# Performance work log

Measured on AMD Instinct MI355X. Metric: run time of the kernel, lower is better.

The kernel has to match this reference:

```python
import jax, jax.numpy as jnp
import numpy as np

LEAK = 0.01  # torch LeakyReLU default negative_slope

def lrelu(x):
    return jnp.where(x >= 0, x, LEAK * x)

def edge_conv(x, src, dst, ea, W1, b1, W2, b2):
    # message: cat(x_i=target, x_j=source, edge_attr) -> Linear -> LeakyReLU -> Linear
    m = jnp.concatenate([x[dst], x[src], ea], axis=1)          # [E, 2F+Fe]
    h = lrelu(m @ W1 + b1) @ W2 + b2                            # [E, H]
    n = x.shape[0]
    agg = jnp.full((n, h.shape[1]), jnp.inf, h.dtype).at[dst].min(h)  # scatter-min at target
    return jnp.where(jnp.isfinite(agg), agg, jnp.zeros_like(agg))     # empty nodes -> 0


def setup_inputs() -> dict:
    key = jax.random.key(0)
    ks = jax.random.split(key, 20)
    B, N, E = 4, 20000, 640000
    NF, AD, EF, H = 2, 1, 1, 8
    inp = {
        "node_features": jax.random.randint(ks[0], (B, N, NF), 0, 10, dtype=jnp.int32),
        "actions": jax.random.normal(ks[1], (B, N), dtype=jnp.float32),
        "edge_index": jax.random.randint(ks[2], (B, 2, E), 0, N, dtype=jnp.int64),
        "edge_features": jax.random.normal(ks[3], (B, E, EF), dtype=jnp.float32),
    }
    d0 = NF + AD  # 3
    def lin(k, fin, fout):
        s = 1.0 / np.sqrt(fin)
        k1, k2 = jax.random.split(k)
        return (jax.random.uniform(k1, (fin, fout), jnp.float32, -s, s),
                jax.random.uniform(k2, (fout,), jnp.float32, -s, s))
    inp["c1_W1"], inp["c1_b1"] = lin(ks[4], 2 * d0 + EF, H)
    inp["c1_W2"], inp["c1_b2"] = lin(ks[5], H, H)
    inp["c2_W1"], inp["c2_b1"] = lin(ks[6], 2 * H + 1, H)
    inp["c2_W2"], inp["c2_b2"] = lin(ks[7], H, H)
    inp["c3_W1"], inp["c3_b1"] = lin(ks[8], 2 * H + 1, H)
    inp["c3_W2"], inp["c3_b2"] = lin(ks[9], H, H)
    inp["lin_W"], inp["lin_b"] = lin(ks[10], d0 + H, 1)
    return inp


def reference(node_features, actions, edge_index, edge_features,
              c1_W1, c1_b1, c1_W2, c1_b2,
              c2_W1, c2_b1, c2_W2, c2_b2,
              c3_W1, c3_b1, c3_W2, c3_b2,
              lin_W, lin_b):
    # x = int(node_features) concat actions  -> float
    x0 = jnp.concatenate([node_features.astype(jnp.int32).astype(jnp.float32),
                          actions[..., None]], axis=-1)  # [B,N,3]

    def per_graph(x0g, eig, eag):
        src, dst = eig[0], eig[1]  # flow source_to_target: x_j=src, x_i=dst
        h = lrelu(edge_conv(x0g, src, dst, eag, c1_W1, c1_b1, c1_W2, c1_b2))
        h = lrelu(edge_conv(h, src, dst, eag, c2_W1, c2_b1, c2_W2, c2_b2))
        h = lrelu(edge_conv(h, src, dst, eag, c3_W1, c3_b1, c3_W2, c3_b2))
        xc = jnp.concatenate([x0g, h], axis=1)  # [N, 3+8]
        return jnp.sum(xc, axis=0)              # sum-pool over nodes

    pooled = jax.vmap(per_graph)(x0, edge_index, edge_features)  # [B, 11]
    return pooled @ lin_W + lin_b  # [B, 1]
```

## Files before the change

kernel.cpp:

```cpp
#include <hip/hip_runtime.h>

#define LEAK 0.01f
#define BS 128
#define PCHUNK 4096
#define PT 512
#define CT 256
#define MAXNB 256
#define CPGMAX 256

__device__ __forceinline__ float lrelu(float v) {
    return v >= 0.f ? v : LEAK * v;
}

__device__ __forceinline__ unsigned int fmin_encode(float x) {
    unsigned int u = __float_as_uint(x);
    return (u & 0x80000000u) ? ~u : (u | 0x80000000u);
}
__device__ __forceinline__ float fmin_decode(unsigned int k) {
    unsigned int u = (k & 0x80000000u) ? (k ^ 0x80000000u) : ~k;
    return __uint_as_float(u);
}

__device__ __forceinline__ void block_add(float c, float* dst) {
    __shared__ float wsum[8];
#pragma unroll
    for (int off = 32; off > 0; off >>= 1) c += __shfl_down(c, off, 64);
    int lane = threadIdx.x & 63;
    int wave = threadIdx.x >> 6;
    if (lane == 0) wsum[wave] = c;
    __syncthreads();
    if (threadIdx.x == 0) {
        float s = 0.f;
        int nw = blockDim.x >> 6;
        for (int w = 0; w < nw; ++w) s += wsum[w];
        atomicAdd(dst, s);
    }
}

__global__ __launch_bounds__(PT) void part_init_kernel(
    const int* __restrict__ ei, const float* __restrict__ ea,
    int2* __restrict__ pairs, int* __restrict__ ofs,
    const int* __restrict__ nf, const float* __restrict__ act,
    const float* __restrict__ W1, const float* __restrict__ b1,
    const float* __restrict__ lw, const float* __restrict__ lb,
    float* __restrict__ a1, float* __restrict__ a2, float* __restrict__ out,
    int E, int N, int NB, int CPG) {
    int b = blockIdx.y;
    int t = threadIdx.x;

    if (blockIdx.x >= CPG) {
        int n = (blockIdx.x - CPG) * PT + t;
        float c = 0.f;
        if (n < N) {
            size_t i = (size_t)b * N + n;
            float x0 = (float)nf[i * 2 + 0];
            float x1 = (float)nf[i * 2 + 1];
            float x2 = act[i];
            float v1[8], v2[8];
#pragma unroll
            for (int j = 0; j < 8; ++j) {
                v1[j] = b1[j] + x0 * W1[0 * 8 + j] + x1 * W1[1 * 8 + j] + x2 * W1[2 * 8 + j];
                v2[j] =         x0 * W1[3 * 8 + j] + x1 * W1[4 * 8 + j] + x2 * W1[5 * 8 + j];
            }
            float4* o1 = (float4*)(a1 + i * 8);
            float4* o2 = (float4*)(a2 + i * 8);
            o1[0] = make_float4(v1[0], v1[1], v1[2], v1[3]);
            o1[1] = make_float4(v1[4], v1[5], v1[6], v1[7]);
            o2[0] = make_float4(v2[0], v2[1], v2[2], v2[3]);
            o2[1] = make_float4(v2[4], v2[5], v2[6], v2[7]);
            c = x0 * lw[0] + x1 * lw[1] + x2 * lw[2];
            if (n == 0) c += lb[0];
        }
        block_add(c, &out[b]);
        return;
    }

    __shared__ int lc[MAXNB];
    __shared__ int lofs[MAXNB + 1];
    __shared__ int ts[PT];
    int c = blockIdx.x;
    for (int i = t; i < NB; i += PT) lc[i] = 0;
    __syncthreads();

    int e0 = c * PCHUNK;
    int end = min(e0 + PCHUNK, E);
    const int* srow = ei + (size_t)b * 2 * E;
    const int* drow = srow + E;

    int pk[PCHUNK / PT];
#pragma unroll
    for (int j = 0; j < PCHUNK / PT; ++j) {
        int e = e0 + j * PT + t;
        int p = -1;
        if (e < end) {
            int d = drow[e];
            int bin = d >> 7;
            int r = atomicAdd(&lc[bin], 1);
            p = bin | ((d & 127) << 10) | (r << 17);
        }
        pk[j] = p;
    }
    __syncthreads();

    int v = (t < NB) ? lc[t] : 0;
    ts[t] = v;
    __syncthreads();
    int incl = v;
    for (int off = 1; off < PT; off <<= 1) {
        int add = (t >= off) ? ts[t - off] : 0;
        __syncthreads();
        incl += add;
        ts[t] = incl;
        __syncthreads();
    }
    if (t < NB) lofs[t] = incl - v;
    if (t == PT - 1) lofs[NB] = incl;
    __syncthreads();

    for (int i = t; i <= NB; i += PT) {
        int w = lofs[i];
        ofs[((size_t)b * (NB + 1) + i) * CPG + c] = w;
        if (i < NB) lc[i] = w;
    }
    __syncthreads();

    size_t pbase = (size_t)b * E + e0;
#pragma unroll
    for (int j = 0; j < PCHUNK / PT; ++j) {
        int e = e0 + j * PT + t;
        if (e < end) {
            int p = pk[j];
            int bin = p & 1023;
            int dl = (p >> 10) & 127;
            int r = p >> 17;
            int pos = lc[bin] + r;
            pairs[pbase + pos] =
                make_int2(srow[e] | (dl << 16), __float_as_int(ea[(size_t)b * E + e]));
        }
    }
}


__device__ __forceinline__ void conv_edge_body(
    const float* __restrict__ a2g, const float* we, const float* bb,
    const float* __restrict__ W2, int2 p,
    const float* __restrict__ a1s, unsigned int* __restrict__ acc) {
    int srcn = p.x & 0xFFFF;
    int dl = (p.x >> 16) & 127;
    float eav = __int_as_float(p.y);
    const float4* q = (const float4*)(a2g + (size_t)srcn * 8);
    float4 lo = q[0], hi = q[1];
    float h1[8];
    h1[0] = a1s[dl * 9 + 0] + lo.x; h1[1] = a1s[dl * 9 + 1] + lo.y;
    h1[2] = a1s[dl * 9 + 2] + lo.z; h1[3] = a1s[dl * 9 + 3] + lo.w;
    h1[4] = a1s[dl * 9 + 4] + hi.x; h1[5] = a1s[dl * 9 + 5] + hi.y;
    h1[6] = a1s[dl * 9 + 6] + hi.z; h1[7] = a1s[dl * 9 + 7] + hi.w;
#pragma unroll
    for (int j = 0; j < 8; ++j) {
        h1[j] = fmaf(eav, we[j], h1[j]);
        h1[j] = lrelu(h1[j]);
    }
    float h2[8];
#pragma unroll
    for (int j = 0; j < 8; ++j) h2[j] = bb[j];
#pragma unroll
    for (int kk = 0; kk < 8; ++kk) {
        float hk = h1[kk];
#pragma unroll
        for (int j = 0; j < 8; ++j) h2[j] = fmaf(hk, W2[kk * 8 + j], h2[j]);
    }
#pragma unroll
    for (int j = 0; j < 8; ++j)
        atomicMin(&acc[dl * 9 + j], fmin_encode(h2[j]));
}

__device__ __forceinline__ void conv_edges_runs(
    const float* __restrict__ a2g, const float* we, const float* bb,
    const float* __restrict__ W2, const int2* __restrict__ pairsg,
    const int* __restrict__ ofb, int CPG,
    const float* __restrict__ a1s, unsigned int* __restrict__ acc,
    int* __restrict__ rs, int* __restrict__ re) {
    int t = threadIdx.x;
    for (int c = t; c < CPG; c += CT) {
        rs[c] = ofb[c];
        re[c] = ofb[CPG + c];
    }
    __syncthreads();
    int sw = t >> 5, sub = t & 31;
    const int nsw = CT >> 5;
    int c = sw;
    int2 pcur = make_int2(0, 0);
    int kcur = 0, k1cur = 0;
    if (c < CPG) {
        int cb = c * PCHUNK;
        kcur = cb + rs[c] + sub;
        k1cur = cb + re[c];
        if (kcur < k1cur) pcur = pairsg[kcur];
    }
    while (c < CPG) {
        int cn = c + nsw;
        int2 pnext = make_int2(0, 0);
        int knext = 0, k1next = 0;
        if (cn < CPG) {
            int cb = cn * PCHUNK;
            knext = cb + rs[cn] + sub;
            k1next = cb + re[cn];
            if (knext < k1next) pnext = pairsg[knext];
        }
        if (kcur < k1cur) {
            conv_edge_body(a2g, we, bb, W2, pcur, a1s, acc);
            for (int k = kcur + 32; k < k1cur; k += 32)
                conv_edge_body(a2g, we, bb, W2, pairsg[k], a1s, acc);
        }
        c = cn; kcur = knext; k1cur = k1next; pcur = pnext;
    }
}

__global__ __launch_bounds__(CT) void conv_mid_kernel(
    const float* __restrict__ a1, const float* __restrict__ a2,
    const float* __restrict__ w1e, const float* __restrict__ W2,
    const float* __restrict__ b2,
    const float* __restrict__ nW1, const float* __restrict__ nb1,
    const int* __restrict__ ofs, const int2* __restrict__ pairs,
    float* __restrict__ na1, float* __restrict__ na2,
    int N, int NB, int CPG, int E) {
    __shared__ float a1s[BS * 9];
    __shared__ unsigned int acc[BS * 9];
    __shared__ int rs[CPGMAX];
    __shared__ int re[CPGMAX];
    int b = blockIdx.y;
    int bin = blockIdx.x;
    int n0 = bin << 7;
    int nCnt = min(BS, N - n0);
    int t = threadIdx.x;
    size_t gn0 = ((size_t)b * N + n0) * 8;

    for (int i = t; i < nCnt * 8; i += CT)
        a1s[(i >> 3) * 9 + (i & 7)] = a1[gn0 + i];
    for (int i = t; i < BS * 9; i += CT) acc[i] = 0xFFFFFFFFu;
    float we[8], bb[8];
#pragma unroll
    for (int j = 0; j < 8; ++j) { we[j] = w1e[j]; bb[j] = b2[j]; }
    __syncthreads();

    conv_edges_runs(a2 + (size_t)b * N * 8, we, bb, W2,
                    pairs + (size_t)b * E,
                    ofs + ((size_t)b * (NB + 1) + bin) * CPG,
                    CPG, a1s, acc, rs, re);
    __syncthreads();

    for (int i = t; i < nCnt * 8; i += CT) {
        float v = fmin_decode(acc[(i >> 3) * 9 + (i & 7)]);
        unsigned int u = __float_as_uint(v);
        if ((u & 0x7F800000u) == 0x7F800000u) v = 0.f;
        a1s[(i >> 3) * 9 + (i & 7)] = lrelu(v);
    }
    __syncthreads();

    for (int nh = t; nh < nCnt * 2; nh += CT) {
        int node = nh >> 1, half = nh & 1;
        float h[8];
#pragma unroll
        for (int j = 0; j < 8; ++j) h[j] = a1s[node * 9 + j];
        float v[8];
#pragma unroll
        for (int j = 0; j < 8; ++j) v[j] = half ? 0.f : nb1[j];
        const float* Wbase = nW1 + (half ? 64 : 0);
#pragma unroll
        for (int k = 0; k < 8; ++k) {
            float hk = h[k];
#pragma unroll
            for (int j = 0; j < 8; ++j) v[j] = fmaf(hk, Wbase[k * 8 + j], v[j]);
        }
        float* dst = (half ? na2 : na1) + gn0 + (size_t)node * 8;
        float4* o = (float4*)dst;
        o[0] = make_float4(v[0], v[1], v[2], v[3]);
        o[1] = make_float4(v[4], v[5], v[6], v[7]);
    }
}

__global__ __launch_bounds__(CT) void conv_final_kernel(
    const float* __restrict__ a1, const float* __restrict__ a2,
    const float* __restrict__ w1e, const float* __restrict__ W2,
    const float* __restrict__ b2, const float* __restrict__ lw,
    const int* __restrict__ ofs, const int2* __restrict__ pairs,
    float* __restrict__ out, int N, int NB, int CPG, int E) {
    __shared__ float a1s[BS * 9];
    __shared__ unsigned int acc[BS * 9];
    __shared__ int rs[CPGMAX];
    __shared__ int re[CPGMAX];
    int b = blockIdx.y;
    int bin = blockIdx.x;
    int n0 = bin << 7;
    int nCnt = min(BS, N - n0);
    int t = threadIdx.x;
    size_t gn0 = ((size_t)b * N + n0) * 8;

    for (int i = t; i < nCnt * 8; i += CT)
        a1s[(i >> 3) * 9 + (i & 7)] = a1[gn0 + i];
    for (int i = t; i < BS * 9; i += CT) acc[i] = 0xFFFFFFFFu;
    float we[8], bb[8];
#pragma unroll
    for (int j = 0; j < 8; ++j) { we[j] = w1e[j]; bb[j] = b2[j]; }
    __syncthreads();

    conv_edges_runs(a2 + (size_t)b * N * 8, we, bb, W2,
                    pairs + (size_t)b * E,
                    ofs + ((size_t)b * (NB + 1) + bin) * CPG,
                    CPG, a1s, acc, rs, re);
    __syncthreads();

    float c = 0.f;
    if (t < nCnt) {
#pragma unroll
        for (int j = 0; j < 8; ++j) {
            float v = fmin_decode(acc[t * 9 + j]);
            unsigned int u = __float_as_uint(v);
            if ((u & 0x7F800000u) == 0x7F800000u) v = 0.f;
            c = fmaf(lrelu(v), lw[3 + j], c);
        }
    }
    __syncthreads();
    block_add(c, &out[b]);
}


__global__ __launch_bounds__(256) void node_init_kernel(
    const int* __restrict__ nf, const float* __restrict__ act,
    float* __restrict__ x0, int BN) {
    int tid = blockIdx.x * blockDim.x + threadIdx.x;
    if (tid >= BN) return;
    x0[tid * 3 + 0] = (float)nf[tid * 2 + 0];
    x0[tid * 3 + 1] = (float)nf[tid * 2 + 1];
    x0[tid * 3 + 2] = act[tid];
}

template <int D>
__global__ __launch_bounds__(256) void edge_conv_kernel(
    const float* __restrict__ x, const int* __restrict__ ei,
    const float* __restrict__ ea,
    const float* __restrict__ W1, const float* __restrict__ b1,
    const float* __restrict__ W2, const float* __restrict__ b2,
    unsigned int* __restrict__ agg, int E, int N, int B) {
    int tid = blockIdx.x * blockDim.x + threadIdx.x;
    if (tid >= B * E) return;
    int b = tid / E;
    int e = tid - b * E;
    const int* eb = ei + (size_t)b * 2 * E;
    int s = eb[e];
    int d = eb[E + e];
    const float* xi = x + ((size_t)b * N + d) * D;
    const float* xj = x + ((size_t)b * N + s) * D;
    constexpr int M = 2 * D + 1;
    float m[M];
#pragma unroll
    for (int k = 0; k < D; ++k) { m[k] = xi[k]; m[D + k] = xj[k]; }
    m[2 * D] = ea[(size_t)b * E + e];
    float h1[8];
#pragma unroll
    for (int j = 0; j < 8; ++j) h1[j] = b1[j];
#pragma unroll
    for (int k = 0; k < M; ++k) {
        float mk = m[k];
#pragma unroll
        for (int j = 0; j < 8; ++j) h1[j] = fmaf(mk, W1[k * 8 + j], h1[j]);
    }
#pragma unroll
    for (int j = 0; j < 8; ++j) h1[j] = lrelu(h1[j]);
    float h2[8];
#pragma unroll
    for (int j = 0; j < 8; ++j) h2[j] = b2[j];
#pragma unroll
    for (int k = 0; k < 8; ++k) {
        float hk = h1[k];
#pragma unroll
        for (int j = 0; j < 8; ++j) h2[j] = fmaf(hk, W2[k * 8 + j], h2[j]);
    }
    unsigned int* ag = agg + ((size_t)b * N + d) * 8;
#pragma unroll
    for (int j = 0; j < 8; ++j) atomicMin(&ag[j], fmin_encode(h2[j]));
}

__global__ __launch_bounds__(256) void finalize_kernel(
    unsigned int* __restrict__ agg, int total) {
    int tid = blockIdx.x * blockDim.x + threadIdx.x;
    if (tid >= total) return;
    float v = fmin_decode(agg[tid]);
    unsigned int u = __float_as_uint(v);
    if ((u & 0x7F800000u) == 0x7F800000u) v = 0.f;
    ((float*)agg)[tid] = lrelu(v);
}

__global__ __launch_bounds__(256) void pool_kernel(
    const float* __restrict__ x0, const float* __restrict__ h,
    const float* __restrict__ lw, const float* __restrict__ lb,
    float* __restrict__ out, int N) {
    int b = blockIdx.y;
    int n = blockIdx.x * blockDim.x + threadIdx.x;
    float c = 0.f;
    if (n < N) {
        const float* x = x0 + ((size_t)b * N + n) * 3;
        const float* hh = h + ((size_t)b * N + n) * 8;
        c = x[0] * lw[0] + x[1] * lw[1] + x[2] * lw[2];
#pragma unroll
        for (int k = 0; k < 8; ++k) c = fmaf(hh[k], lw[3 + k], c);
        if (n == 0) c += lb[0];
    }
    block_add(c, &out[b]);
}


static inline size_t align256(size_t x) { return (x + 255) & ~(size_t)255; }

extern "C" void kernel_launch(void* const* d_in, const int* in_sizes, int n_in,
                              void* d_out, int out_size, void* d_ws, size_t ws_size,
                              hipStream_t stream) {
    const int B = 4;
    const int N = in_sizes[1] / B;
    const int E = in_sizes[2] / (2 * B);

    const int*   nf  = (const int*)d_in[0];
    const float* act = (const float*)d_in[1];
    const int*   ei  = (const int*)d_in[2];
    const float* ea  = (const float*)d_in[3];
    const float* c1_W1 = (const float*)d_in[4];
    const float* c1_b1 = (const float*)d_in[5];
    const float* c1_W2 = (const float*)d_in[6];
    const float* c1_b2 = (const float*)d_in[7];
    const float* c2_W1 = (const float*)d_in[8];
    const float* c2_b1 = (const float*)d_in[9];
    const float* c2_W2 = (const float*)d_in[10];
    const float* c2_b2 = (const float*)d_in[11];
    const float* c3_W1 = (const float*)d_in[12];
    const float* c3_b1 = (const float*)d_in[13];
    const float* c3_W2 = (const float*)d_in[14];
    const float* c3_b2 = (const float*)d_in[15];
    const float* lw    = (const float*)d_in[16];
    const float* lb    = (const float*)d_in[17];
    float* out = (float*)d_out;

    const int BN = B * N;
    const int BE = B * E;
    const int NB = (N + BS - 1) / BS;
    const int CPG = (E + PCHUNK - 1) / PCHUNK;

    char* ws = (char*)d_ws;
    size_t off = 0;
    float* a1A  = (float*)(ws + off);  off += align256((size_t)BN * 8 * 4);
    float* a2A  = (float*)(ws + off);  off += align256((size_t)BN * 8 * 4);
    float* a1B  = (float*)(ws + off);  off += align256((size_t)BN * 8 * 4);
    float* a2B  = (float*)(ws + off);  off += align256((size_t)BN * 8 * 4);
    int* ofs    = (int*)(ws + off);    off += align256((size_t)B * (NB + 1) * CPG * 4);
    int2* pairs = (int2*)(ws + off);   off += align256((size_t)BE * 8);
    float* x0   = (float*)(ws + off);  off += align256((size_t)BN * 3 * 4);
    const bool useFast = (off <= ws_size) && (NB <= MAXNB) && (CPG <= CPGMAX) &&
                         (N <= 32768);

    hipMemsetAsync(out, 0, (size_t)B * sizeof(float), stream);

    if (useFast) {
        const int initBlocks = (N + PT - 1) / PT;
        dim3 pgrid(CPG + initBlocks, B);
        dim3 cgrid(NB, B);

        part_init_kernel<<<pgrid, PT, 0, stream>>>(
            ei, ea, pairs, ofs, nf, act, c1_W1, c1_b1, lw, lb,
            a1A, a2A, out, E, N, NB, CPG);

        conv_mid_kernel<<<cgrid, CT, 0, stream>>>(
            a1A, a2A, c1_W1 + 6 * 8, c1_W2, c1_b2, c2_W1, c2_b1,
            ofs, pairs, a1B, a2B, N, NB, CPG, E);
        conv_mid_kernel<<<cgrid, CT, 0, stream>>>(
            a1B, a2B, c2_W1 + 16 * 8, c2_W2, c2_b2, c3_W1, c3_b1,
            ofs, pairs, a1A, a2A, N, NB, CPG, E);
        conv_final_kernel<<<cgrid, CT, 0, stream>>>(
            a1A, a2A, c3_W1 + 16 * 8, c3_W2, c3_b2, lw,
            ofs, pairs, out, N, NB, CPG, E);
    } else {
        const int egrid = (BE + 255) / 256;
        const int aggTotal = BN * 8;
        const int agrid = (aggTotal + 255) / 256;
        const size_t aggBytes = (size_t)aggTotal * 4;
        unsigned int* uA = (unsigned int*)a1A;
        unsigned int* uB = (unsigned int*)a1B;

        node_init_kernel<<<(BN + 255) / 256, 256, 0, stream>>>(nf, act, x0, BN);

        hipMemsetAsync(uA, 0xFF, aggBytes, stream);
        edge_conv_kernel<3><<<egrid, 256, 0, stream>>>(
            x0, ei, ea, c1_W1, c1_b1, c1_W2, c1_b2, uA, E, N, B);
        finalize_kernel<<<agrid, 256, 0, stream>>>(uA, aggTotal);

        hipMemsetAsync(uB, 0xFF, aggBytes, stream);
        edge_conv_kernel<8><<<egrid, 256, 0, stream>>>(
            (const float*)uA, ei, ea, c2_W1, c2_b1, c2_W2, c2_b2, uB, E, N, B);
        finalize_kernel<<<agrid, 256, 0, stream>>>(uB, aggTotal);

        hipMemsetAsync(uA, 0xFF, aggBytes, stream);
        edge_conv_kernel<8><<<egrid, 256, 0, stream>>>(
            (const float*)uB, ei, ea, c3_W1, c3_b1, c3_W2, c3_b2, uA, E, N, B);
        finalize_kernel<<<agrid, 256, 0, stream>>>(uA, aggTotal);

        dim3 plgrid((N + 255) / 256, B);
        pool_kernel<<<plgrid, 256, 0, stream>>>(x0, (const float*)uA, lw, lb, out, N);
    }
}
```

Baseline: 221.0 us.

## Store source-side projections in bf16 and double conv block size

The per-node source projection (a2) is now stored as packed bf16, halving the bytes of the random gather done for every edge. The edge loop also loads the next run's a2 row together with its pair record, so the gather is prefetched. CT is raised from 256 to 512 threads per block to put more waves on each bin. The trade-off is lost precision in the gathered values, and larger blocks may lower occupancy or add shared-memory atomic contention.

```diff
diff --git a/kernel.cpp b/kernel.cpp
--- a/kernel.cpp
+++ b/kernel.cpp
@@ -4,7 +4,7 @@
 #define BS 128
 #define PCHUNK 4096
 #define PT 512
-#define CT 256
+#define CT 512
 #define MAXNB 256
 #define CPGMAX 256
 
@@ -19,6 +19,11 @@
 __device__ __forceinline__ float fmin_decode(unsigned int k) {
     unsigned int u = (k & 0x80000000u) ? (k ^ 0x80000000u) : ~k;
     return __uint_as_float(u);
+}
+
+__device__ __forceinline__ unsigned int bf16_rne(float f) {
+    unsigned int u = __float_as_uint(f);
+    return (u + 0x7FFFu + ((u >> 16) & 1u)) >> 16;
 }
 
 __device__ __forceinline__ void block_add(float c, float* dst) {
@@ -43,8 +48,8 @@
     const int* __restrict__ nf, const float* __restrict__ act,
     const float* __restrict__ W1, const float* __restrict__ b1,
     const float* __restrict__ lw, const float* __restrict__ lb,
-    float* __restrict__ a1, float* __restrict__ a2, float* __restrict__ out,
-    int E, int N, int NB, int CPG) {
+    float* __restrict__ a1, unsigned short* __restrict__ a2,
+    float* __restrict__ out, int E, int N, int NB, int CPG) {
     int b = blockIdx.y;
     int t = threadIdx.x;
 
@@ -63,11 +68,13 @@
                 v2[j] =         x0 * W1[3 * 8 + j] + x1 * W1[4 * 8 + j] + x2 * W1[5 * 8 + j];
             }
             float4* o1 = (float4*)(a1 + i * 8);
-            float4* o2 = (float4*)(a2 + i * 8);
             o1[0] = make_float4(v1[0], v1[1], v1[2], v1[3]);
             o1[1] = make_float4(v1[4], v1[5], v1[6], v1[7]);
-            o2[0] = make_float4(v2[0], v2[1], v2[2], v2[3]);
-            o2[1] = make_float4(v2[4], v2[5], v2[6], v2[7]);
+            unsigned int w[4];
+#pragma unroll
+            for (int q = 0; q < 4; ++q)
+                w[q] = bf16_rne(v2[2 * q]) | (bf16_rne(v2[2 * q + 1]) << 16);
+            *(int4*)(a2 + i * 8) = make_int4(w[0], w[1], w[2], w[3]);
             c = x0 * lw[0] + x1 * lw[1] + x2 * lw[2];
             if (n == 0) c += lb[0];
         }
@@ -141,22 +148,24 @@
 }
 
 
-__device__ __forceinline__ void conv_edge_body(
-    const float* __restrict__ a2g, const float* we, const float* bb,
-    const float* __restrict__ W2, int2 p,
-    const float* __restrict__ a1s, unsigned int* __restrict__ acc) {
-    int srcn = p.x & 0xFFFF;
+__device__ __forceinline__ void conv_edge_compute(
+    const float* we, const float* bb, const float* __restrict__ W2,
+    int2 p, int4 raw, const float* __restrict__ a1s,
+    unsigned int* __restrict__ acc) {
     int dl = (p.x >> 16) & 127;
     float eav = __int_as_float(p.y);
-    const float4* q = (const float4*)(a2g + (size_t)srcn * 8);
-    float4 lo = q[0], hi = q[1];
+    unsigned int wq[4] = {(unsigned int)raw.x, (unsigned int)raw.y,
+                          (unsigned int)raw.z, (unsigned int)raw.w};
+    float a2v[8];
+#pragma unroll
+    for (int q = 0; q < 4; ++q) {
+        a2v[2 * q]     = __uint_as_float(wq[q] << 16);
+        a2v[2 * q + 1] = __uint_as_float(wq[q] & 0xFFFF0000u);
+    }
     float h1[8];
-    h1[0] = a1s[dl * 9 + 0] + lo.x; h1[1] = a1s[dl * 9 + 1] + lo.y;
-    h1[2] = a1s[dl * 9 + 2] + lo.z; h1[3] = a1s[dl * 9 + 3] + lo.w;
-    h1[4] = a1s[dl * 9 + 4] + hi.x; h1[5] = a1s[dl * 9 + 5] + hi.y;
-    h1[6] = a1s[dl * 9 + 6] + hi.z; h1[7] = a1s[dl * 9 + 7] + hi.w;
 #pragma unroll
     for (int j = 0; j < 8; ++j) {
+        h1[j] = a1s[dl * 9 + j] + a2v[j];
         h1[j] = fmaf(eav, we[j], h1[j]);
         h1[j] = lrelu(h1[j]);
     }
@@ -175,7 +184,7 @@
 }
 
 __device__ __forceinline__ void conv_edges_runs(
-    const float* __restrict__ a2g, const float* we, const float* bb,
+    const unsigned short* __restrict__ a2g, const float* we, const float* bb,
     const float* __restrict__ W2, const int2* __restrict__ pairsg,
     const int* __restrict__ ofb, int CPG,
     const float* __restrict__ a1s, unsigned int* __restrict__ acc,
@@ -190,39 +199,55 @@
     const int nsw = CT >> 5;
     int c = sw;
     int2 pcur = make_int2(0, 0);
+    int4 vcur = make_int4(0, 0, 0, 0);
     int kcur = 0, k1cur = 0;
+    bool haveCur = false;
     if (c < CPG) {
         int cb = c * PCHUNK;
         kcur = cb + rs[c] + sub;
         k1cur = cb + re[c];
-        if (kcur < k1cur) pcur = pairsg[kcur];
+        if (kcur < k1cur) {
+            pcur = pairsg[kcur];
+            vcur = *(const int4*)(a2g + (size_t)(pcur.x & 0xFFFF) * 8);
+            haveCur = true;
+        }
     }
     while (c < CPG) {
         int cn = c + nsw;
         int2 pnext = make_int2(0, 0);
+        int4 vnext = make_int4(0, 0, 0, 0);
         int knext = 0, k1next = 0;
+        bool haveNext = false;
         if (cn < CPG) {
             int cb = cn * PCHUNK;
             knext = cb + rs[cn] + sub;
             k1next = cb + re[cn];
-            if (knext < k1next) pnext = pairsg[knext];
-        }
-        if (kcur < k1cur) {
-            conv_edge_body(a2g, we, bb, W2, pcur, a1s, acc);
-            for (int k = kcur + 32; k < k1cur; k += 32)
-                conv_edge_body(a2g, we, bb, W2, pairsg[k], a1s, acc);
-        }
-        c = cn; kcur = knext; k1cur = k1next; pcur = pnext;
+            if (knext < k1next) {
+                pnext = pairsg[knext];
+                vnext = *(const int4*)(a2g + (size_t)(pnext.x & 0xFFFF) * 8);
+                haveNext = true;
+            }
+        }
+        if (haveCur) {
+            conv_edge_compute(we, bb, W2, pcur, vcur, a1s, acc);
+            for (int k = kcur + 32; k < k1cur; k += 32) {
+                int2 p = pairsg[k];
+                int4 v = *(const int4*)(a2g + (size_t)(p.x & 0xFFFF) * 8);
+                conv_edge_compute(we, bb, W2, p, v, a1s, acc);
+            }
+        }
+        c = cn; pcur = pnext; vcur = vnext; kcur = knext; k1cur = k1next;
+        haveCur = haveNext;
     }
 }
 
 __global__ __launch_bounds__(CT) void conv_mid_kernel(
-    const float* __restrict__ a1, const float* __restrict__ a2,
+    const float* __restrict__ a1, const unsigned short* __restrict__ a2,
     const float* __restrict__ w1e, const float* __restrict__ W2,
     const float* __restrict__ b2,
     const float* __restrict__ nW1, const float* __restrict__ nb1,
     const int* __restrict__ ofs, const int2* __restrict__ pairs,
-    float* __restrict__ na1, float* __restrict__ na2,
+    float* __restrict__ na1, unsigned short* __restrict__ na2,
     int N, int NB, int CPG, int E) {
     __shared__ float a1s[BS * 9];
     __shared__ unsigned int acc[BS * 9];
@@ -233,10 +258,10 @@
     int n0 = bin << 7;
     int nCnt = min(BS, N - n0);
     int t = threadIdx.x;
-    size_t gn0 = ((size_t)b * N + n0) * 8;
+    size_t node0 = (size_t)b * N + n0;
 
     for (int i = t; i < nCnt * 8; i += CT)
-        a1s[(i >> 3) * 9 + (i & 7)] = a1[gn0 + i];
+        a1s[(i >> 3) * 9 + (i & 7)] = a1[node0 * 8 + i];
     for (int i = t; i < BS * 9; i += CT) acc[i] = 0xFFFFFFFFu;
     float we[8], bb[8];
 #pragma unroll
@@ -272,15 +297,22 @@
 #pragma unroll
             for (int j = 0; j < 8; ++j) v[j] = fmaf(hk, Wbase[k * 8 + j], v[j]);
         }
-        float* dst = (half ? na2 : na1) + gn0 + (size_t)node * 8;
-        float4* o = (float4*)dst;
-        o[0] = make_float4(v[0], v[1], v[2], v[3]);
-        o[1] = make_float4(v[4], v[5], v[6], v[7]);
+        if (half) {
+            unsigned int w[4];
+#pragma unroll
+            for (int q = 0; q < 4; ++q)
+                w[q] = bf16_rne(v[2 * q]) | (bf16_rne(v[2 * q + 1]) << 16);
+            *(int4*)(na2 + (node0 + node) * 8) = make_int4(w[0], w[1], w[2], w[3]);
+        } else {
+            float4* o = (float4*)(na1 + (node0 + node) * 8);
+            o[0] = make_float4(v[0], v[1], v[2], v[3]);
+            o[1] = make_float4(v[4], v[5], v[6], v[7]);
+        }
     }
 }
 
 __global__ __launch_bounds__(CT) void conv_final_kernel(
-    const float* __restrict__ a1, const float* __restrict__ a2,
+    const float* __restrict__ a1, const unsigned short* __restrict__ a2,
     const float* __restrict__ w1e, const float* __restrict__ W2,
     const float* __restrict__ b2, const float* __restrict__ lw,
     const int* __restrict__ ofs, const int2* __restrict__ pairs,
@@ -294,10 +326,10 @@
     int n0 = bin << 7;
     int nCnt = min(BS, N - n0);
     int t = threadIdx.x;
-    size_t gn0 = ((size_t)b * N + n0) * 8;
+    size_t node0 = (size_t)b * N + n0;
 
     for (int i = t; i < nCnt * 8; i += CT)
-        a1s[(i >> 3) * 9 + (i & 7)] = a1[gn0 + i];
+        a1s[(i >> 3) * 9 + (i & 7)] = a1[node0 * 8 + i];
     for (int i = t; i < BS * 9; i += CT) acc[i] = 0xFFFFFFFFu;
     float we[8], bb[8];
 #pragma unroll
@@ -446,10 +478,10 @@
 
     char* ws = (char*)d_ws;
     size_t off = 0;
-    float* a1A  = (float*)(ws + off);  off += align256((size_t)BN * 8 * 4);
-    float* a2A  = (float*)(ws + off);  off += align256((size_t)BN * 8 * 4);
-    float* a1B  = (float*)(ws + off);  off += align256((size_t)BN * 8 * 4);
-    float* a2B  = (float*)(ws + off);  off += align256((size_t)BN * 8 * 4);
+    float* a1A = (float*)(ws + off);           off += align256((size_t)BN * 8 * 4);
+    float* a1B = (float*)(ws + off);           off += align256((size_t)BN * 8 * 4);
+    unsigned short* a2A = (unsigned short*)(ws + off); off += align256((size_t)BN * 8 * 2);
+    unsigned short* a2B = (unsigned short*)(ws + off); off += align256((size_t)BN * 8 * 2);
     int* ofs    = (int*)(ws + off);    off += align256((size_t)B * (NB + 1) * CPG * 4);
     int2* pairs = (int2*)(ws + off);   off += align256((size_t)BE * 8);
     float* x0   = (float*)(ws + off);  off += align256((size_t)BN * 3 * 4);
```

Result: no change. 219.7 us (-0.6%).
